# Kernel tuning notes

Hardware: AMD Instinct MI355X
Metric: run time of the kernel (lower is better)

Reference implementation:

```python
import jax, jax.numpy as jnp
import numpy as np

NUM_CLASSES = 19
W_CE, W_DICE, W_FOCAL, W_LOVASZ = 1.0, 1.0, 1.0, 0.5
GAMMA, ALPHA = 2.0, 0.25
SMOOTH = 1e-8


def setup_inputs() -> dict:
    key = jax.random.key(0)
    k1, k2 = jax.random.split(key)
    outputs = jax.random.normal(k1, (4, NUM_CLASSES, 512, 1024), dtype=jnp.float32)
    masks = jax.random.randint(k2, (4, 512, 1024), 0, NUM_CLASSES, dtype=jnp.int64)
    return {"outputs": outputs, "masks": masks}


def _ce_and_focal(outputs, masks):
    # per-pixel target log-prob, shape [B,H,W]
    logp = jax.nn.log_softmax(outputs, axis=1)
    logpt = jnp.take_along_axis(logp, masks[:, None], axis=1)[:, 0]
    ce = -jnp.mean(logpt)
    pt = jnp.exp(logpt)
    focal = jnp.mean(-ALPHA * (1.0 - pt) ** GAMMA * logpt)
    return ce, focal


def _dice(outputs, masks):
    probs = jax.nn.softmax(outputs, axis=1)  # [B,C,H,W]
    onehot = (masks[:, None] == jnp.arange(NUM_CLASSES)[None, :, None, None]).astype(jnp.float32)
    inter = jnp.sum(probs * onehot, axis=(0, 2, 3))       # [C]
    union = jnp.sum(probs, axis=(0, 2, 3)) + jnp.sum(onehot, axis=(0, 2, 3))
    present = jnp.sum(onehot, axis=(0, 2, 3)) > 0
    dice_pc = (2.0 * inter + SMOOTH) / (union + SMOOTH)
    n_present = jnp.sum(present.astype(jnp.float32))
    dice_avg = jnp.sum(jnp.where(present, dice_pc, 0.0)) / jnp.maximum(n_present, 1.0)
    return jnp.where(n_present > 0, 1.0 - dice_avg, 1.0)


def _lovasz(outputs, masks):
    B, C, H, W = outputs.shape
    lg = jnp.transpose(outputs, (1, 0, 2, 3)).reshape(C, -1)  # [C,N] logits per class
    fg = (masks.reshape(-1)[None, :] == jnp.arange(C)[:, None]).astype(jnp.float32)  # [C,N]
    sgn = 2.0 * fg - 1.0
    errs = 1.0 - lg * sgn
    idx = jnp.argsort(-errs, axis=1)                  # descending sort order
    sorted_errs = jnp.take_along_axis(errs, idx, axis=1)
    sorted_fg = jnp.take_along_axis(fg, idx, axis=1)
    err_cumm = jnp.cumsum(sorted_fg, axis=1)
    opp_cumm = jnp.cumsum(1.0 - sorted_fg, axis=1)
    err = jnp.sum(sorted_fg, axis=1, keepdims=True)
    grad = 1.0 - (err - err_cumm) / (err + opp_cumm)
    grad = jnp.concatenate([grad[:, :1], grad[:, 1:] - grad[:, :-1]], axis=1)
    per_class = jnp.sum(jax.nn.relu(sorted_errs) * grad, axis=1)  # [C]
    present = jnp.sum(fg, axis=1) > 0
    return jnp.sum(jnp.where(present, per_class, 0.0)) / C


def reference(outputs, masks):
    ce, focal = _ce_and_focal(outputs, masks)
    dice = _dice(outputs, masks)
    lov = _lovasz(outputs, masks)
    return W_CE * ce + W_DICE * dice + W_FOCAL * focal + W_LOVASZ * lov
```

## Files before the change

kernel.cpp:

```cpp
#include <hip/hip_runtime.h>
#include <hip/hip_fp16.h>

#define HW (512 * 1024)
#define NPIX (4 * HW)
#define NCLS 19
#define NB 256
#define BSCALE 32.0f
#define L2E 1.4426950408889634f
#define LN2 0.6931471805599453f

#define NTHR 256
#define NBLK 1024
#define ITERS 4

#define ACC_BYTES 512
#define HIST_ENTRIES (NCLS * NB)
#define NREP 2

__global__ __launch_bounds__(NTHR, 4) void k_main(const float* __restrict__ lg,
                                                  const int* __restrict__ masks,
                                                  unsigned* __restrict__ gHist,
                                                  double* __restrict__ acc) {
    __shared__ unsigned hist[HIST_ENTRIES];
    __shared__ float sInter[NCLS];
    __shared__ unsigned sCnt[NCLS];
    __shared__ float sSumP[NCLS];
    __shared__ float sCE, sFocal;
    int tid = threadIdx.x;
    for (int k = tid; k < HIST_ENTRIES; k += NTHR) hist[k] = 0u;
    if (tid < NCLS) { sInter[tid] = 0.f; sCnt[tid] = 0u; sSumP[tid] = 0.f; }
    if (tid == 0) { sCE = 0.f; sFocal = 0.f; }
    __syncthreads();

    float sumP[NCLS];
#pragma unroll
    for (int c = 0; c < NCLS; ++c) sumP[c] = 0.f;
    float ceAcc = 0.f, foAcc = 0.f;

    int base2 = blockIdx.x * (NTHR * ITERS);
    for (int it = 0; it < ITERS; ++it) {
        int i2 = base2 + it * NTHR + tid;
        int pix = i2 * 2;
        int b = pix >> 19;
        int hw = pix & (HW - 1);
        const float* lp = lg + (((size_t)(b * NCLS)) << 19) + hw;
        int2 tt = *reinterpret_cast<const int2*>(masks + pix);
        int t0 = tt.x, t1 = tt.y;

        float S0 = 0.f, S1 = 0.f;
        float lt0 = 0.f, lt1 = 0.f;
        __half2 ph[NCLS];
#pragma unroll
        for (int c = 0; c < NCLS; ++c) {
            float2 x = *reinterpret_cast<const float2*>(lp + (((size_t)c) << 19));
            bool f0 = (c == t0), f1 = (c == t1);
            float e0 = f0 ? (1.f - x.x) : (1.f + x.x);
            float e1 = f1 ? (1.f - x.y) : (1.f + x.y);
            if (e0 > 0.f) {
                int k = (int)(e0 * BSCALE);
                k = (k < NB) ? k : (NB - 1);
                atomicAdd(&hist[c * NB + k], f0 ? 1u : 0x10001u);
            }
            if (e1 > 0.f) {
                int k = (int)(e1 * BSCALE);
                k = (k < NB) ? k : (NB - 1);
                atomicAdd(&hist[c * NB + k], f1 ? 1u : 0x10001u);
            }
            if (f0) lt0 = x.x;
            if (f1) lt1 = x.y;
            float p0 = exp2f(x.x * L2E);
            float p1 = exp2f(x.y * L2E);
            S0 += p0; S1 += p1;
            ph[c] = __floats2half2_rn(p0, p1);
        }

        float inv0 = 1.f / S0, inv1 = 1.f / S1;
#pragma unroll
        for (int c = 0; c < NCLS; ++c) {
            float2 p = __half22float2(ph[c]);
            sumP[c] += p.x * inv0 + p.y * inv1;
        }

        float logpt0 = lt0 - log2f(S0) * LN2;
        float logpt1 = lt1 - log2f(S1) * LN2;
        float pt0 = exp2f(lt0 * L2E) * inv0;
        float pt1 = exp2f(lt1 * L2E) * inv1;
        ceAcc -= logpt0 + logpt1;
        float om0 = 1.f - pt0, om1 = 1.f - pt1;
        foAcc -= 0.25f * (om0 * om0 * logpt0 + om1 * om1 * logpt1);
        atomicAdd(&sInter[t0], pt0);
        atomicAdd(&sInter[t1], pt1);
        atomicAdd(&sCnt[t0], 1u);
        atomicAdd(&sCnt[t1], 1u);
    }

    int lane = tid & 63;
#pragma unroll
    for (int c = 0; c < NCLS; ++c) {
        float v = sumP[c];
#pragma unroll
        for (int s = 32; s > 0; s >>= 1) v += __shfl_xor(v, s);
        if (lane == 0) atomicAdd(&sSumP[c], v);
    }
    {
        float v = ceAcc, w = foAcc;
#pragma unroll
        for (int s = 32; s > 0; s >>= 1) { v += __shfl_xor(v, s); w += __shfl_xor(w, s); }
        if (lane == 0) { atomicAdd(&sCE, v); atomicAdd(&sFocal, w); }
    }
    __syncthreads();

    unsigned* gh = gHist + (blockIdx.x & (NREP - 1)) * HIST_ENTRIES;
    for (int k = tid; k < HIST_ENTRIES; k += NTHR) {
        unsigned v = hist[k];
        if (v) atomicAdd(&gh[k], v);
    }
    if (tid < NCLS) {
        atomicAdd(&acc[2 + tid], (double)sInter[tid]);
        atomicAdd(&acc[21 + tid], (double)sSumP[tid]);
        atomicAdd(&acc[40 + tid], (double)sCnt[tid]);
    }
    if (tid == 0) {
        atomicAdd(&acc[0], (double)sCE);
        atomicAdd(&acc[1], (double)sFocal);
    }
}

__global__ __launch_bounds__(320) void k_scan_combine(const unsigned* __restrict__ gHist,
                                                      const double* __restrict__ acc,
                                                      float* __restrict__ outv) {
    int tid = threadIdx.x;
    int lane = tid & 63;
    int wave = tid >> 6;
    __shared__ double wsum[5];
    double lov = 0.0;

    for (int r = 0; r < 4; ++r) {
        int c = r * 5 + wave;
        if (c < NCLS) {
            unsigned a[4], bgc[4];
            unsigned cn = 0, cb = 0;
#pragma unroll
            for (int j = 0; j < 4; ++j) {
                int k = c * NB + lane * 4 + j;
                unsigned v0 = gHist[k];
                unsigned v1 = gHist[HIST_ENTRIES + k];
                a[j] = (v0 & 0xFFFFu) + (v1 & 0xFFFFu);
                bgc[j] = (v0 >> 16) + (v1 >> 16);
                cn += a[j];
                cb += bgc[j];
            }
            unsigned ninc = cn, binc = cb;
#pragma unroll
            for (int s = 1; s < 64; s <<= 1) {
                unsigned tn = __shfl_down(ninc, s, 64);
                unsigned tb = __shfl_down(binc, s, 64);
                if (lane + s < 64) { ninc += tn; binc += tb; }
            }
            double n = (double)(ninc - cn);
            double B = (double)(binc - cb);
            double P = acc[40 + c];
            if (P > 0.5) {
#pragma unroll
                for (int j = 3; j >= 0; --j) {
                    if (a[j]) {
                        double ad = (double)a[j], bd = (double)bgc[j];
                        double Gend = (n + ad) / (P + B + bd);
                        double Gstart = n / (P + B);
                        double emid = ((double)(lane * 4 + j) + 0.5) / 32.0;
                        lov += emid * (Gend - Gstart);
                        n += ad;
                        B += bd;
                    }
                }
            }
        }
    }
#pragma unroll
    for (int s = 32; s > 0; s >>= 1) lov += __shfl_xor(lov, s);
    if (lane == 0) wsum[wave] = lov;
    __syncthreads();

    if (tid == 0) {
        double L = 0.0;
        for (int w = 0; w < 5; ++w) L += wsum[w];
        double ce = acc[0] / (double)NPIX;
        double fo = acc[1] / (double)NPIX;
        double dsum = 0.0, npres = 0.0;
        for (int c = 0; c < NCLS; ++c) {
            double cnt = acc[40 + c];
            if (cnt > 0.5) {
                double inter = acc[2 + c];
                double uni = acc[21 + c] + cnt;
                dsum += (2.0 * inter + 1e-8) / (uni + 1e-8);
                npres += 1.0;
            }
        }
        double dice = (npres > 0.0) ? (1.0 - dsum / npres) : 1.0;
        outv[0] = (float)(ce + fo + dice + 0.5 * (L / (double)NCLS));
    }
}

extern "C" void kernel_launch(void* const* d_in, const int* in_sizes, int n_in,
                              void* d_out, int out_size, void* d_ws, size_t ws_size,
                              hipStream_t stream) {
    const float* lg = (const float*)d_in[0];
    const int* masks = (const int*)d_in[1];
    float* outv = (float*)d_out;

    char* ws = (char*)d_ws;
    double* acc = (double*)ws;
    unsigned* gHist = (unsigned*)(ws + ACC_BYTES);

    hipMemsetAsync(d_ws, 0, ACC_BYTES + (size_t)NREP * HIST_ENTRIES * 4, stream);

    k_main<<<NBLK, NTHR, 0, stream>>>(lg, masks, gHist, acc);
    k_scan_combine<<<1, 320, 0, stream>>>(gHist, acc, outv);
}
```

Measured before the change: 292.3 us.

## Prefetch all class logits, keep fp32 probs, pack inter/count into double atomics

Loads all 19 class logit pairs up front so the memory requests are issued together, and keeps the exp values in fp32 registers instead of half precision. The per-pixel intersection and count shared atomics are merged into one double atomic that encodes the count as an offset, and the offset is decoded at block end. The launch doubles the block count with half the iterations per block, drops the occupancy hint from launch bounds, and uses four global histogram replicas to spread contention. The cost is higher register pressure, possibly lower occupancy, and double-precision shared atomics, which may be slow.

```diff
diff --git a/kernel.cpp b/kernel.cpp
--- a/kernel.cpp
+++ b/kernel.cpp
@@ -1,5 +1,4 @@
 #include <hip/hip_runtime.h>
-#include <hip/hip_fp16.h>
 
 #define HW (512 * 1024)
 #define NPIX (4 * HW)
@@ -10,25 +9,25 @@
 #define LN2 0.6931471805599453f
 
 #define NTHR 256
-#define NBLK 1024
-#define ITERS 4
+#define NBLK 2048
+#define ITERS 2
 
 #define ACC_BYTES 512
 #define HIST_ENTRIES (NCLS * NB)
-#define NREP 2
-
-__global__ __launch_bounds__(NTHR, 4) void k_main(const float* __restrict__ lg,
-                                                  const int* __restrict__ masks,
-                                                  unsigned* __restrict__ gHist,
-                                                  double* __restrict__ acc) {
+#define NREP 4
+#define CNT_OFF 1048576.0
+
+__global__ __launch_bounds__(NTHR) void k_main(const float* __restrict__ lg,
+                                               const int* __restrict__ masks,
+                                               unsigned* __restrict__ gHist,
+                                               double* __restrict__ acc) {
     __shared__ unsigned hist[HIST_ENTRIES];
-    __shared__ float sInter[NCLS];
-    __shared__ unsigned sCnt[NCLS];
+    __shared__ double sIC[NCLS];
     __shared__ float sSumP[NCLS];
     __shared__ float sCE, sFocal;
     int tid = threadIdx.x;
     for (int k = tid; k < HIST_ENTRIES; k += NTHR) hist[k] = 0u;
-    if (tid < NCLS) { sInter[tid] = 0.f; sCnt[tid] = 0u; sSumP[tid] = 0.f; }
+    if (tid < NCLS) { sIC[tid] = 0.0; sSumP[tid] = 0.f; }
     if (tid == 0) { sCE = 0.f; sFocal = 0.f; }
     __syncthreads();
 
@@ -47,15 +46,19 @@
         int2 tt = *reinterpret_cast<const int2*>(masks + pix);
         int t0 = tt.x, t1 = tt.y;
 
+        float2 l[NCLS];
+#pragma unroll
+        for (int c = 0; c < NCLS; ++c)
+            l[c] = *reinterpret_cast<const float2*>(lp + (((size_t)c) << 19));
+
         float S0 = 0.f, S1 = 0.f;
         float lt0 = 0.f, lt1 = 0.f;
-        __half2 ph[NCLS];
 #pragma unroll
         for (int c = 0; c < NCLS; ++c) {
-            float2 x = *reinterpret_cast<const float2*>(lp + (((size_t)c) << 19));
+            float x0 = l[c].x, x1 = l[c].y;
             bool f0 = (c == t0), f1 = (c == t1);
-            float e0 = f0 ? (1.f - x.x) : (1.f + x.x);
-            float e1 = f1 ? (1.f - x.y) : (1.f + x.y);
+            float e0 = f0 ? (1.f - x0) : (1.f + x0);
+            float e1 = f1 ? (1.f - x1) : (1.f + x1);
             if (e0 > 0.f) {
                 int k = (int)(e0 * BSCALE);
                 k = (k < NB) ? k : (NB - 1);
@@ -66,20 +69,17 @@
                 k = (k < NB) ? k : (NB - 1);
                 atomicAdd(&hist[c * NB + k], f1 ? 1u : 0x10001u);
             }
-            if (f0) lt0 = x.x;
-            if (f1) lt1 = x.y;
-            float p0 = exp2f(x.x * L2E);
-            float p1 = exp2f(x.y * L2E);
+            if (f0) lt0 = x0;
+            if (f1) lt1 = x1;
+            float p0 = exp2f(x0 * L2E);
+            float p1 = exp2f(x1 * L2E);
             S0 += p0; S1 += p1;
-            ph[c] = __floats2half2_rn(p0, p1);
+            l[c].x = p0; l[c].y = p1;
         }
 
         float inv0 = 1.f / S0, inv1 = 1.f / S1;
 #pragma unroll
-        for (int c = 0; c < NCLS; ++c) {
-            float2 p = __half22float2(ph[c]);
-            sumP[c] += p.x * inv0 + p.y * inv1;
-        }
+        for (int c = 0; c < NCLS; ++c) sumP[c] += l[c].x * inv0 + l[c].y * inv1;
 
         float logpt0 = lt0 - log2f(S0) * LN2;
         float logpt1 = lt1 - log2f(S1) * LN2;
@@ -88,10 +88,8 @@
         ceAcc -= logpt0 + logpt1;
         float om0 = 1.f - pt0, om1 = 1.f - pt1;
         foAcc -= 0.25f * (om0 * om0 * logpt0 + om1 * om1 * logpt1);
-        atomicAdd(&sInter[t0], pt0);
-        atomicAdd(&sInter[t1], pt1);
-        atomicAdd(&sCnt[t0], 1u);
-        atomicAdd(&sCnt[t1], 1u);
+        atomicAdd(&sIC[t0], (double)pt0 + CNT_OFF);
+        atomicAdd(&sIC[t1], (double)pt1 + CNT_OFF);
     }
 
     int lane = tid & 63;
@@ -116,9 +114,12 @@
         if (v) atomicAdd(&gh[k], v);
     }
     if (tid < NCLS) {
-        atomicAdd(&acc[2 + tid], (double)sInter[tid]);
+        double s = sIC[tid];
+        double n = floor(s / CNT_OFF);
+        double inter = s - n * CNT_OFF;
+        atomicAdd(&acc[2 + tid], inter);
         atomicAdd(&acc[21 + tid], (double)sSumP[tid]);
-        atomicAdd(&acc[40 + tid], (double)sCnt[tid]);
+        atomicAdd(&acc[40 + tid], n);
     }
     if (tid == 0) {
         atomicAdd(&acc[0], (double)sCE);
@@ -143,12 +144,17 @@
 #pragma unroll
             for (int j = 0; j < 4; ++j) {
                 int k = c * NB + lane * 4 + j;
-                unsigned v0 = gHist[k];
-                unsigned v1 = gHist[HIST_ENTRIES + k];
-                a[j] = (v0 & 0xFFFFu) + (v1 & 0xFFFFu);
-                bgc[j] = (v0 >> 16) + (v1 >> 16);
-                cn += a[j];
-                cb += bgc[j];
+                unsigned at = 0, bt = 0;
+#pragma unroll
+                for (int r2 = 0; r2 < NREP; ++r2) {
+                    unsigned v = gHist[r2 * HIST_ENTRIES + k];
+                    at += v & 0xFFFFu;
+                    bt += v >> 16;
+                }
+                a[j] = at;
+                bgc[j] = bt;
+                cn += at;
+                cb += bt;
             }
             unsigned ninc = cn, binc = cb;
 #pragma unroll
```

New measurement: 294.0 us. Within noise of the previous version (+0.6%).
